# Kernel tuning notes

Measured on AMD Instinct MI355X. Metric: run time of the kernel, lower is better.

## Reference

```python
import jax, jax.numpy as jnp
import numpy as np

B, L, H, V, P = 256, 16, 256, 5000, 4
NPG, DEG, STEPS, OUT = 150, 4, 4, 2000
N, E = B * NPG, B * NPG * DEG


def _seg_softmax(x, seg, num):
    # sparse softmax over variable-size groups (rows of the sparse matrix)
    m = jax.ops.segment_max(x, seg, num_segments=num)
    e = jnp.exp(x - m[seg])
    s = jax.ops.segment_sum(e, seg, num_segments=num)
    return e / s[seg]


def setup_inputs():
    key = jax.random.key(0)
    ks = jax.random.split(key, 24)
    questions = jax.random.normal(ks[0], (B, L, H), jnp.float32)
    lengths = jax.random.randint(ks[1], (B,), L // 2, L + 1)
    node_attrs = jax.random.normal(ks[2], (N, P - 1, H), jnp.float32)
    edge_attrs = jax.random.normal(ks[3], (E, H), jnp.float32)
    node_graph = jnp.repeat(jnp.arange(B), NPG)
    edge_graph = jnp.repeat(jnp.arange(B), NPG * DEG)
    off = jnp.repeat(jnp.arange(B) * NPG, NPG * DEG)
    edge_src = jax.random.randint(ks[4], (E,), 0, NPG) + off
    edge_dst = jax.random.randint(ks[5], (E,), 0, NPG) + off
    s = float(1.0 / np.sqrt(H))
    u = lambda k, shape: jax.random.uniform(k, shape, jnp.float32, -s, s)
    vocab = jax.random.normal(ks[6], (V, H), jnp.float32) * 0.1
    default_embed = jax.random.uniform(ks[7], (H,), jnp.float32)
    W_norm = jnp.eye(H, dtype=jnp.float32)
    lstm_Wih, lstm_Whh = u(ks[8], (4 * H, H)), u(ks[9], (4 * H, H))
    lstm_bih, lstm_bhh = u(ks[10], (4 * H,)), u(ks[11], (4 * H,))
    rnn_Wih, rnn_Whh = u(ks[12], (H, H)), u(ks[13], (H, H))
    rnn_bih, rnn_bhh = u(ks[14], (H,)), u(ks[15], (H,))
    prop_embeds = jax.random.normal(ks[16], (P, H), jnp.float32) * 0.1
    Ws_property = jax.random.uniform(ks[17], (P, H, H), jnp.float32) * s
    W_state = jax.random.uniform(ks[18], (H,), jnp.float32) * s
    W_relation = jax.random.uniform(ks[19], (H,), jnp.float32) * s
    lin_W, lin_b = u(ks[20], (OUT, 2 * H)), u(ks[21], (OUT,))
    return dict(questions=questions, node_attrs=node_attrs, edge_attrs=edge_attrs,
                vocab=vocab, default_embed=default_embed, W_norm=W_norm,
                lstm_Wih=lstm_Wih, lstm_Whh=lstm_Whh, lstm_bih=lstm_bih, lstm_bhh=lstm_bhh,
                rnn_Wih=rnn_Wih, rnn_Whh=rnn_Whh, rnn_bih=rnn_bih, rnn_bhh=rnn_bhh,
                prop_embeds=prop_embeds, Ws_property=Ws_property,
                W_state=W_state, W_relation=W_relation, lin_W=lin_W, lin_b=lin_b,
                lengths=lengths, node_graph=node_graph, edge_graph=edge_graph,
                edge_src=edge_src, edge_dst=edge_dst)


def reference(questions, node_attrs, edge_attrs, vocab, default_embed, W_norm,
              lstm_Wih, lstm_Whh, lstm_bih, lstm_bhh,
              rnn_Wih, rnn_Whh, rnn_bih, rnn_bhh,
              prop_embeds, Ws_property, W_state, W_relation, lin_W, lin_b,
              lengths, node_graph, edge_graph, edge_src, edge_dst):
    # ---- NormalizeWordsModel (tagger) ----
    words = questions.reshape(B * L, H)
    C = jnp.concatenate([vocab, default_embed[None]], axis=0)  # [V+1, H]
    Pm = jax.nn.softmax((words @ W_norm) @ C.T, axis=1)        # [B*L, V+1]
    Vtag = Pm[:, -1:] * words + Pm[:, :-1] @ vocab             # [B*L, H]
    Vpad = Vtag.reshape(B, L, H)

    # ---- LSTM encoder: final hidden at last valid step (packed-sequence semantics) ----
    valid = jnp.arange(L)[:, None] < lengths[None, :]  # [L, B]

    def lstm_step(carry, inp):
        h, c = carry
        x, v = inp
        g = x @ lstm_Wih.T + lstm_bih + h @ lstm_Whh.T + lstm_bhh
        i, f, gc, o = jnp.split(g, 4, axis=-1)  # torch gate order i,f,g,o
        c_new = jax.nn.sigmoid(f) * c + jax.nn.sigmoid(i) * jnp.tanh(gc)
        h_new = jax.nn.sigmoid(o) * jnp.tanh(c_new)
        vm = v[:, None]
        return (jnp.where(vm, h_new, h), jnp.where(vm, c_new, c)), None

    z = jnp.zeros((B, H), questions.dtype)
    (Q, _), _ = jax.lax.scan(lstm_step, (z, z), (Vpad.transpose(1, 0, 2), valid))

    # ---- InstructionsDecoder: relu RNNCell fed the same Q each step ----
    def dec_step(hx, _):
        hx = jax.nn.relu(Q @ rnn_Wih.T + rnn_bih + hx @ rnn_Whh.T + rnn_bhh)
        return hx, hx

    _, Hins = jax.lax.scan(dec_step, z, None, length=STEPS)
    Hins = Hins.transpose(1, 0, 2)  # [B, STEPS, H]

    # ---- attention over (masked) tagged words ----
    att = jnp.einsum('bnh,blh->bnl', Hins, Vpad)
    mask = jnp.arange(L)[None, None, :] < lengths[:, None, None]
    att = jnp.where(mask, att, -jnp.inf)
    R = jax.nn.softmax(att, axis=-1) @ Vpad  # instructions [B, STEPS, H]

    # ---- NSMCell recurrence ----
    nodes_per_graph = jax.ops.segment_sum(jnp.ones(N, questions.dtype), node_graph, num_segments=B)
    dist = (1.0 / nodes_per_graph)[node_graph]  # [N]
    prop_sim = None
    for step in range(STEPS):
        instr = R[:, step]  # [B, H]
        prop_sim = jax.nn.softmax(instr @ prop_embeds.T, axis=1)  # [B, P]
        transformed = jnp.einsum('phk,npk->nph', Ws_property[:-1], node_attrs)  # [N, P-1, H]
        node_scores = jax.nn.elu(jnp.sum(
            prop_sim[node_graph, :-1, None] * instr[node_graph, None, :] * transformed, axis=1))  # [N, H]
        edge_scores = jax.nn.elu(instr[edge_graph] * (edge_attrs @ Ws_property[-1].T))  # [E, H]
        p_state = _seg_softmax(node_scores @ W_state, node_graph, B)  # [N]
        agg = jax.ops.segment_sum(dist[edge_src, None] * edge_scores, edge_dst, num_segments=N)  # [N, H]
        p_rel = _seg_softmax(agg @ W_relation, node_graph, B)  # [N]
        r = prop_sim[node_graph, -1]
        dist = r * p_rel + (1.0 - r) * p_state

    # ---- readout ----
    node_feat = jnp.sum(prop_sim[node_graph, :-1, None] * node_attrs, axis=1)  # [N, H]
    aggregated = jax.ops.segment_sum(dist[:, None] * node_feat, node_graph, num_segments=B)  # [B, H]
    return jnp.concatenate([Q, aggregated], axis=1) @ lin_W.T + lin_b
```

## Files before the change

### kernel.cpp

```cpp
#include <hip/hip_runtime.h>
#include <hip/hip_bf16.h>
#include <math.h>

#define BB 256
#define LL 16
#define HH 256
#define VV 5000
#define NPG 150
#define DEG 4
#define NSTEPS 4
#define OUTD 2000
#define NN (BB*NPG)
#define EE (BB*NPG*DEG)
#define BL (BB*LL)
#define VPAD 5120
#define KPAD 5024

__device__ __forceinline__ float wred_sum(float v){
  #pragma unroll
  for(int o=32;o;o>>=1) v += __shfl_down(v,o,64);
  return v;
}
__device__ __forceinline__ float wred_max(float v){
  #pragma unroll
  for(int o=32;o;o>>=1) v = fmaxf(v,__shfl_down(v,o,64));
  return v;
}
__device__ __forceinline__ float block_sum256(float v, float* sh){
  v = wred_sum(v);
  __syncthreads();
  if((threadIdx.x&63)==0) sh[threadIdx.x>>6]=v;
  __syncthreads();
  return sh[0]+sh[1]+sh[2]+sh[3];
}
__device__ __forceinline__ float block_max256(float v, float* sh){
  v = wred_max(v);
  __syncthreads();
  if((threadIdx.x&63)==0) sh[threadIdx.x>>6]=v;
  __syncthreads();
  return fmaxf(fmaxf(sh[0],sh[1]),fmaxf(sh[2],sh[3]));
}
__device__ __forceinline__ float eluf(float x){ return x>0.f ? x : expm1f(x); }
__device__ __forceinline__ float sigf(float x){ return 1.f/(1.f+expf(-x)); }
__device__ __forceinline__ float b2f(unsigned short s){
  union{float f; unsigned int u;} x; x.u = ((unsigned int)s)<<16; return x.f;
}
__device__ __forceinline__ unsigned short f2bf_bits(float x){
  union { __hip_bfloat16 h; unsigned short s; } u; u.h = __float2bfloat16(x); return u.s;
}

__device__ __forceinline__ void async16(void* lds, const void* g){
  __builtin_amdgcn_global_load_lds(
      (const __attribute__((address_space(1))) unsigned int*)g,
      (__attribute__((address_space(3))) unsigned int*)lds, 16, 0, 0);
}

typedef __attribute__((ext_vector_type(8))) short short8;
typedef __attribute__((ext_vector_type(4))) float f32x4;

__device__ __forceinline__ short8 pack8(float4 a, float4 b){
  short8 r;
  r[0]=(short)f2bf_bits(a.x); r[1]=(short)f2bf_bits(a.y);
  r[2]=(short)f2bf_bits(a.z); r[3]=(short)f2bf_bits(a.w);
  r[4]=(short)f2bf_bits(b.x); r[5]=(short)f2bf_bits(b.y);
  r[6]=(short)f2bf_bits(b.z); r[7]=(short)f2bf_bits(b.w);
  return r;
}

template<int EPI>
__global__ __launch_bounds__(256) void mfma_bt_bf16_k(
    const __hip_bfloat16* __restrict__ A, const __hip_bfloat16* __restrict__ Bt,
    float* __restrict__ Cf, __hip_bfloat16* __restrict__ Cb,
    int lda, int ldb, int ldc, int Nreal,
    int kItersTotal, int kPerSplit, const float* __restrict__ bias,
    const float* __restrict__ rscale)
{
  __shared__ __hip_bfloat16 As[128*32];
  __shared__ __hip_bfloat16 Bs[128*32];
  const int bm = blockIdx.y*128, bn = blockIdx.x*128;
  const int tid = threadIdx.x;
  int k0 = blockIdx.z * kPerSplit;
  int k1 = k0 + kPerSplit; if (k1 > kItersTotal) k1 = kItersTotal;
  const int lane = tid & 63, wave = tid >> 6;
  const int quad = lane >> 4, r16 = lane & 15;
  const int wr = wave >> 1, wc = wave & 1;
  f32x4 acc[4][4] = {};
  const int c0 = tid, c1 = tid + 256;
  const int ar0 = c0 >> 2, ak0 = (c0 & 3)*8;
  const int ar1 = c1 >> 2, ak1 = (c1 & 3)*8;
  const __hip_bfloat16* Ab = A + (size_t)bm*lda;
  const __hip_bfloat16* Bb = Bt + (size_t)bn*ldb;
  for (int kk = k0; kk < k1; ++kk){
    const int kb = kk*32;
    async16(&As[c0*8], Ab + (size_t)ar0*lda + kb + ak0);
    async16(&As[c1*8], Ab + (size_t)ar1*lda + kb + ak1);
    async16(&Bs[c0*8], Bb + (size_t)ar0*ldb + kb + ak0);
    async16(&Bs[c1*8], Bb + (size_t)ar1*ldb + kb + ak1);
    __syncthreads();
    short8 av[4], bv[4];
    #pragma unroll
    for (int i=0;i<4;i++){
      av[i] = *(const short8*)&As[(wr*64 + i*16 + r16)*32 + quad*8];
      bv[i] = *(const short8*)&Bs[(wc*64 + i*16 + r16)*32 + quad*8];
    }
    #pragma unroll
    for (int i=0;i<4;i++)
      #pragma unroll
      for (int j=0;j<4;j++)
        acc[i][j] = __builtin_amdgcn_mfma_f32_16x16x32_bf16(av[i], bv[j], acc[i][j], 0,0,0);
    __syncthreads();
  }
  #pragma unroll
  for (int i=0;i<4;i++){
    int row = bm + wr*64 + i*16 + quad*4;
    #pragma unroll
    for (int j=0;j<4;j++){
      int col = bn + wc*64 + j*16 + r16;
      if (col >= Nreal) continue;
      #pragma unroll
      for (int r=0;r<4;r++){
        float v = acc[i][j][r];
        if (EPI==0){ if (bias) v += bias[col]; Cf[(size_t)(row+r)*ldc + col] = v; }
        else if (EPI==1){ Cb[(size_t)(row+r)*ldc + col] = __float2bfloat16(v); }
        else { if (rscale) v *= rscale[row+r]; atomicAdd(&Cf[(size_t)(row+r)*ldc + col], v); }
      }
    }
  }
}

template<int EPI>
__global__ __launch_bounds__(256) void mfma_bt_f32_k(
    const float* __restrict__ A, const float* __restrict__ Bt,
    float* __restrict__ Cf, __hip_bfloat16* __restrict__ Cb,
    int lda, int ldb, int ldc, int Nreal,
    int kIters, const float* __restrict__ bias)
{
  __shared__ __hip_bfloat16 As[128*32];
  __shared__ __hip_bfloat16 Bs[128*32];
  const int bm = blockIdx.y*128, bn = blockIdx.x*128;
  const int tid = threadIdx.x;
  const int lane = tid & 63, wave = tid >> 6;
  const int quad = lane >> 4, r16 = lane & 15;
  const int wr = wave >> 1, wc = wave & 1;
  f32x4 acc[4][4] = {};
  for (int kk = 0; kk < kIters; ++kk){
    const int kb = kk*32;
    #pragma unroll
    for (int i=0;i<2;i++){
      int c = tid + i*256;
      int row = c >> 2, k0 = (c & 3)*8;
      const float* src = A + (size_t)(bm+row)*lda + kb + k0;
      float4 v0 = *(const float4*)(src);
      float4 v1 = *(const float4*)(src+4);
      *(short8*)&As[row*32 + k0] = pack8(v0, v1);
    }
    #pragma unroll
    for (int i=0;i<2;i++){
      int c = tid + i*256;
      int row = c >> 2, k0 = (c & 3)*8;
      float4 v0 = {0.f,0.f,0.f,0.f}, v1 = {0.f,0.f,0.f,0.f};
      if (bn + row < Nreal){
        const float* src = Bt + (size_t)(bn+row)*ldb + kb + k0;
        v0 = *(const float4*)(src);
        v1 = *(const float4*)(src+4);
      }
      *(short8*)&Bs[row*32 + k0] = pack8(v0, v1);
    }
    __syncthreads();
    short8 av[4], bv[4];
    #pragma unroll
    for (int i=0;i<4;i++){
      av[i] = *(const short8*)&As[(wr*64 + i*16 + r16)*32 + quad*8];
      bv[i] = *(const short8*)&Bs[(wc*64 + i*16 + r16)*32 + quad*8];
    }
    #pragma unroll
    for (int i=0;i<4;i++)
      #pragma unroll
      for (int j=0;j<4;j++)
        acc[i][j] = __builtin_amdgcn_mfma_f32_16x16x32_bf16(av[i], bv[j], acc[i][j], 0,0,0);
    __syncthreads();
  }
  #pragma unroll
  for (int i=0;i<4;i++){
    int row = bm + wr*64 + i*16 + quad*4;
    #pragma unroll
    for (int j=0;j<4;j++){
      int col = bn + wc*64 + j*16 + r16;
      if (col >= Nreal) continue;
      #pragma unroll
      for (int r=0;r<4;r++){
        float v = acc[i][j][r];
        if (EPI==0){ if (bias) v += bias[col]; Cf[(size_t)(row+r)*ldc + col] = v; }
        else { Cb[(size_t)(row+r)*ldc + col] = __float2bfloat16(v); }
      }
    }
  }
}

__global__ __launch_bounds__(256) void gemm_exp_k(
    const __hip_bfloat16* __restrict__ A, const __hip_bfloat16* __restrict__ Bt,
    __hip_bfloat16* __restrict__ Pm, float* __restrict__ row_sum,
    float* __restrict__ e_def)
{
  __shared__ __hip_bfloat16 As[128*32];
  __shared__ __hip_bfloat16 Bs[128*32];
  const int bm = blockIdx.y*128, bn = blockIdx.x*128;
  const int tid = threadIdx.x;
  const int lane = tid & 63, wave = tid >> 6;
  const int quad = lane >> 4, r16 = lane & 15;
  const int wr = wave >> 1, wc = wave & 1;
  f32x4 acc[4][4] = {};
  const int c0 = tid, c1 = tid + 256;
  const int ar0 = c0 >> 2, ak0 = (c0 & 3)*8;
  const int ar1 = c1 >> 2, ak1 = (c1 & 3)*8;
  const __hip_bfloat16* Ab = A + (size_t)bm*HH;
  const __hip_bfloat16* Bb = Bt + (size_t)bn*HH;
  for (int kk = 0; kk < HH/32; ++kk){
    const int kb = kk*32;
    async16(&As[c0*8], Ab + (size_t)ar0*HH + kb + ak0);
    async16(&As[c1*8], Ab + (size_t)ar1*HH + kb + ak1);
    async16(&Bs[c0*8], Bb + (size_t)ar0*HH + kb + ak0);
    async16(&Bs[c1*8], Bb + (size_t)ar1*HH + kb + ak1);
    __syncthreads();
    short8 av[4], bv[4];
    #pragma unroll
    for (int i=0;i<4;i++){
      av[i] = *(const short8*)&As[(wr*64 + i*16 + r16)*32 + quad*8];
      bv[i] = *(const short8*)&Bs[(wc*64 + i*16 + r16)*32 + quad*8];
    }
    #pragma unroll
    for (int i=0;i<4;i++)
      #pragma unroll
      for (int j=0;j<4;j++)
        acc[i][j] = __builtin_amdgcn_mfma_f32_16x16x32_bf16(av[i], bv[j], acc[i][j], 0,0,0);
    __syncthreads();
  }
  #pragma unroll
  for (int i=0;i<4;i++){
    int rowb = bm + wr*64 + i*16 + quad*4;
    float rsum[4] = {0.f,0.f,0.f,0.f};
    #pragma unroll
    for (int j=0;j<4;j++){
      int col = bn + wc*64 + j*16 + r16;
      #pragma unroll
      for (int r=0;r<4;r++){
        float e = (col <= VV) ? expf(acc[i][j][r]) : 0.f;
        rsum[r] += e;
        if (col < KPAD) Pm[(size_t)(rowb+r)*KPAD + col] = __float2bfloat16(col < VV ? e : 0.f);
        if (col == VV) e_def[rowb+r] = e;
      }
    }
    #pragma unroll
    for (int r=0;r<4;r++){
      float s = rsum[r];
      s += __shfl_xor(s, 1, 64);
      s += __shfl_xor(s, 2, 64);
      s += __shfl_xor(s, 4, 64);
      s += __shfl_xor(s, 8, 64);
      if (r16 == 0) atomicAdd(&row_sum[rowb+r], s);
    }
  }
}

__global__ __launch_bounds__(1024) void lstm_persist_k(
    const float* __restrict__ gX, const __hip_bfloat16* __restrict__ Whh_bf,
    const int* __restrict__ lengths,
    float* __restrict__ h_out, __hip_bfloat16* __restrict__ hbf_out)
{
  __shared__ __hip_bfloat16 Wl[256*264];
  __shared__ __hip_bfloat16 hbuf[2][16*264];
  __shared__ int len_s[16];
  const int bg = blockIdx.x, tid = threadIdx.x;
  const int lane = tid & 63, w = tid >> 6;
  const int quad = lane >> 4, r16 = lane & 15;
  const int hb = w*16;
  for (int c = tid; c < 8192; c += 1024){
    int row = c >> 5, ci = (c & 31)*8;
    int g = row >> 6, rr = row & 63;
    *(short8*)&Wl[row*264 + ci] = *(const short8*)&Whh_bf[((size_t)(g*256+rr))*256 + ci];
  }
  for (int i = tid; i < 16*264; i += 1024) hbuf[0][i] = __float2bfloat16(0.f);
  if (tid < 16) len_s[tid] = lengths[bg*16 + tid];
  __syncthreads();
  int lenr[4];
  #pragma unroll
  for (int r=0;r<4;r++) lenr[r] = len_s[quad*4 + r];
  f32x4 cstate = {0.f,0.f,0.f,0.f};
  f32x4 hstate = {0.f,0.f,0.f,0.f};
  int p = 0;
  for (int t=0; t<LL; t++){
    f32x4 acc[4] = {};
    const __hip_bfloat16* hr = hbuf[p];
    if (w < 4){
      #pragma unroll
      for (int kc=0; kc<8; kc++){
        short8 a = *(const short8*)&hr[r16*264 + kc*32 + quad*8];
        #pragma unroll
        for (int g=0; g<4; g++){
          short8 b = *(const short8*)&Wl[(g*64 + hb + r16)*264 + kc*32 + quad*8];
          acc[g] = __builtin_amdgcn_mfma_f32_16x16x32_bf16(a, b, acc[g], 0,0,0);
        }
      }
    } else {
      #pragma unroll
      for (int kc=0; kc<8; kc++){
        short8 a = *(const short8*)&hr[r16*264 + kc*32 + quad*8];
        #pragma unroll
        for (int g=0; g<4; g++){
          short8 b = *(const short8*)&Whh_bf[((size_t)(g*256 + hb + r16))*256 + kc*32 + quad*8];
          acc[g] = __builtin_amdgcn_mfma_f32_16x16x32_bf16(a, b, acc[g], 0,0,0);
        }
      }
    }
    #pragma unroll
    for (int r=0;r<4;r++){
      int batch = quad*4 + r;
      const float* gx = gX + ((size_t)((bg*16+batch)*LL + t))*(4*HH) + hb + r16;
      float gi = acc[0][r] + gx[0];
      float gf = acc[1][r] + gx[HH];
      float gc = acc[2][r] + gx[2*HH];
      float go = acc[3][r] + gx[3*HH];
      float cn = sigf(gf)*cstate[r] + sigf(gi)*tanhf(gc);
      float hn = sigf(go)*tanhf(cn);
      if (t < lenr[r]){ cstate[r] = cn; hstate[r] = hn; }
      hbuf[p^1][batch*264 + hb + r16] = __float2bfloat16(hstate[r]);
    }
    p ^= 1;
    __syncthreads();
  }
  #pragma unroll
  for (int r=0;r<4;r++){
    int batch = quad*4 + r;
    size_t o = (size_t)(bg*16+batch)*HH + hb + r16;
    h_out[o] = hstate[r];
    hbf_out[o] = __float2bfloat16(hstate[r]);
  }
}

__global__ __launch_bounds__(1024) void dec_persist_k(
    const __hip_bfloat16* __restrict__ Qbf, const __hip_bfloat16* __restrict__ Wih_bf,
    const __hip_bfloat16* __restrict__ Whh_bf,
    const float* __restrict__ bih, const float* __restrict__ bhh,
    float* __restrict__ Hins)
{
  __shared__ __hip_bfloat16 Wl[256*264];
  __shared__ __hip_bfloat16 xb[2][16*264];
  const int bg = blockIdx.x, tid = threadIdx.x;
  const int lane = tid & 63, w = tid >> 6;
  const int quad = lane >> 4, r16 = lane & 15;
  const int col = w*16 + r16;
  for (int c = tid; c < 8192; c += 1024){
    int row = c >> 5, ci = (c & 31)*8;
    *(short8*)&Wl[row*264 + ci] = *(const short8*)&Whh_bf[(size_t)row*256 + ci];
  }
  f32x4 qp = {};
  #pragma unroll
  for (int kc=0; kc<8; kc++){
    short8 a = *(const short8*)&Qbf[(size_t)(bg*16 + r16)*HH + kc*32 + quad*8];
    short8 b = *(const short8*)&Wih_bf[(size_t)col*HH + kc*32 + quad*8];
    qp = __builtin_amdgcn_mfma_f32_16x16x32_bf16(a, b, qp, 0,0,0);
  }
  const float bihv = bih[col], bhhv = bhh[col];
  __syncthreads();
  #pragma unroll
  for (int r=0;r<4;r++){
    int batch = quad*4 + r;
    float v = fmaxf(qp[r] + bihv + bhhv, 0.f);
    xb[0][batch*264 + col] = __float2bfloat16(v);
    Hins[(size_t)(bg*16+batch)*(NSTEPS*HH) + 0*HH + col] = v;
  }
  __syncthreads();
  int p = 0;
  for (int s=1; s<NSTEPS; s++){
    f32x4 acc = {};
    #pragma unroll
    for (int kc=0; kc<8; kc++){
      short8 a = *(const short8*)&xb[p][r16*264 + kc*32 + quad*8];
      short8 b = *(const short8*)&Wl[col*264 + kc*32 + quad*8];
      acc = __builtin_amdgcn_mfma_f32_16x16x32_bf16(a, b, acc, 0,0,0);
    }
    #pragma unroll
    for (int r=0;r<4;r++){
      int batch = quad*4 + r;
      float v = fmaxf(qp[r] + bihv + acc[r] + bhhv, 0.f);
      xb[p^1][batch*264 + col] = __float2bfloat16(v);
      Hins[(size_t)(bg*16+batch)*(NSTEPS*HH) + s*HH + col] = v;
    }
    p ^= 1;
    __syncthreads();
  }
}

__global__ void cvt_bf16_k(const float* __restrict__ src, __hip_bfloat16* __restrict__ dst, int n){
  int i = (blockIdx.x*256 + threadIdx.x)*4;
  if (i >= n) return;
  float4 v = *(const float4*)(src + i);
  dst[i]   = __float2bfloat16(v.x);
  dst[i+1] = __float2bfloat16(v.y);
  dst[i+2] = __float2bfloat16(v.z);
  dst[i+3] = __float2bfloat16(v.w);
}

__global__ void tr_cvt_k(const float* __restrict__ src, __hip_bfloat16* __restrict__ dst, int R, int Ccols){
  int idx = blockIdx.x*256 + threadIdx.x;
  if (idx >= R*Ccols) return;
  int r = idx / Ccols, c = idx % Ccols;
  dst[(size_t)c*R + r] = __float2bfloat16(src[idx]);
}

__global__ void build_cb_k(const float* __restrict__ vocab, const float* __restrict__ de,
                           __hip_bfloat16* __restrict__ Cb){
  int idx = blockIdx.x*256 + threadIdx.x;
  if (idx >= VPAD*HH) return;
  int v = idx >> 8, h = idx & 255;
  float x = (v < VV) ? vocab[(size_t)v*HH + h] : (v == VV ? de[h] : 0.f);
  Cb[idx] = __float2bfloat16(x);
}

__global__ void build_vt_k(const float* __restrict__ vocab, __hip_bfloat16* __restrict__ VT){
  int idx = blockIdx.x*256 + threadIdx.x;
  if (idx >= HH*KPAD) return;
  int h = idx / KPAD, v = idx % KPAD;
  VT[idx] = __float2bfloat16(v < VV ? vocab[(size_t)v*HH + h] : 0.f);
}

__global__ void bsum_k(const float* a, const float* b, float* o){
  int i = blockIdx.x*256 + threadIdx.x;
  if (i < 4*HH) o[i] = a[i] + b[i];
}

__global__ void init_k(float* dist, float* s_rel){
  int idx = blockIdx.x*256 + threadIdx.x;
  if (idx < NN){ dist[idx] = 1.f/150.f; s_rel[idx] = 0.f; }
}

__global__ void zero_k(float* p, int n){
  int idx = blockIdx.x*256 + threadIdx.x;
  if (idx < n) p[idx] = 0.f;
}

__global__ void inv_k(float* p, int n){
  int idx = blockIdx.x*256 + threadIdx.x;
  if (idx < n) p[idx] = 1.f/p[idx];
}

__global__ void vtag_epi_k(float* __restrict__ Vtag, const float* __restrict__ e_def,
                           const float* __restrict__ inv_s, const float* __restrict__ words){
  int r = blockIdx.x, h = threadIdx.x;
  size_t o = (size_t)r*HH + h;
  Vtag[o] += e_def[r]*inv_s[r]*words[o];
}

__global__ __launch_bounds__(256) void attention_k(const float* __restrict__ Vtag,
                                                   const float* __restrict__ Hins,
                                                   const int* __restrict__ lengths,
                                                   float* __restrict__ R){
  __shared__ float Vl[LL][HH];
  __shared__ float Hn[NSTEPS][HH];
  __shared__ float att[NSTEPS][LL];
  int b = blockIdx.x, tid = threadIdx.x;
  for (int idx=tid; idx<LL*HH; idx+=256){ int l=idx>>8, h=idx&255; Vl[l][h] = Vtag[((size_t)b*LL+l)*HH + h]; }
  for (int idx=tid; idx<NSTEPS*HH; idx+=256){ Hn[idx>>8][idx&255] = Hins[(size_t)b*(NSTEPS*HH) + idx]; }
  __syncthreads();
  if (tid < NSTEPS*LL){
    int n2 = tid>>4, l = tid&15;
    float s = 0.f;
    for (int k=0;k<HH;k++) s += Hn[n2][k]*Vl[l][k];
    att[n2][l] = s;
  }
  __syncthreads();
  int len = lengths[b];
  if (tid < NSTEPS){
    float m = -1e30f;
    for (int l=0;l<len;l++) m = fmaxf(m, att[tid][l]);
    float s = 0.f;
    for (int l=0;l<LL;l++){ float e = (l<len)? expf(att[tid][l]-m) : 0.f; att[tid][l]=e; s+=e; }
    float inv = 1.f/s;
    for (int l=0;l<LL;l++) att[tid][l] *= inv;
  }
  __syncthreads();
  {
    int n2 = tid>>6, h0 = (tid&63)*4;
    float r0=0,r1=0,r2=0,r3=0;
    for (int l=0;l<LL;l++){
      float w = att[n2][l];
      r0 += w*Vl[l][h0]; r1 += w*Vl[l][h0+1]; r2 += w*Vl[l][h0+2]; r3 += w*Vl[l][h0+3];
    }
    float* o = R + (size_t)b*(NSTEPS*HH) + n2*HH + h0;
    o[0]=r0; o[1]=r1; o[2]=r2; o[3]=r3;
  }
}

__global__ __launch_bounds__(256) void prop_sim_all_k(const float* __restrict__ R,
                                                      const float* __restrict__ pe,
                                                      float* __restrict__ psa){
  __shared__ float sp[4];
  int gb = blockIdx.x;
  int s = gb >> 8, b = gb & 255;
  int tid = threadIdx.x;
  int p = tid>>6, lane = tid&63;
  const float* instr = R + (size_t)b*(NSTEPS*HH) + s*HH;
  float v = 0.f;
  for (int h=lane; h<HH; h+=64) v += instr[h]*pe[p*HH+h];
  v = wred_sum(v);
  if (lane==0) sp[p] = v;
  __syncthreads();
  if (tid==0){
    float m = fmaxf(fmaxf(sp[0],sp[1]),fmaxf(sp[2],sp[3]));
    float e0=expf(sp[0]-m), e1=expf(sp[1]-m), e2=expf(sp[2]-m), e3=expf(sp[3]-m);
    float ss = e0+e1+e2+e3;
    float* o = psa + (size_t)s*BB*4 + b*4;
    o[0]=e0/ss; o[1]=e1/ss; o[2]=e2/ss; o[3]=e3/ss;
  }
}

__global__ __launch_bounds__(256) void nsm_scores_k(
    const __hip_bfloat16* __restrict__ Tf, const __hip_bfloat16* __restrict__ ET,
    const float* __restrict__ R, const float* __restrict__ psa_s,
    const float* __restrict__ W_state, const float* __restrict__ Wr,
    const float* __restrict__ dist, const int* __restrict__ esrc, const int* __restrict__ edst,
    float* __restrict__ s_state, float* __restrict__ s_rel, int step)
{
  const int wave = threadIdx.x >> 6, lane = threadIdx.x & 63;
  const int h0 = lane*4;
  if (blockIdx.x < NN/4){
    int n = blockIdx.x*4 + wave;
    int g = n / NPG;
    const float* instr = R + (size_t)g*(NSTEPS*HH) + step*HH;
    float ps0 = psa_s[g*4], ps1 = psa_s[g*4+1], ps2 = psa_s[g*4+2];
    const unsigned short* t = (const unsigned short*)(Tf + (size_t)n*(3*HH));
    ushort4 t0 = *(const ushort4*)(t + h0);
    ushort4 t1 = *(const ushort4*)(t + HH + h0);
    ushort4 t2 = *(const ushort4*)(t + 2*HH + h0);
    float4 iv = *(const float4*)(instr + h0);
    float4 wv = *(const float4*)(W_state + h0);
    float acc;
    acc  = eluf(iv.x*(ps0*b2f(t0.x)+ps1*b2f(t1.x)+ps2*b2f(t2.x)))*wv.x;
    acc += eluf(iv.y*(ps0*b2f(t0.y)+ps1*b2f(t1.y)+ps2*b2f(t2.y)))*wv.y;
    acc += eluf(iv.z*(ps0*b2f(t0.z)+ps1*b2f(t1.z)+ps2*b2f(t2.z)))*wv.z;
    acc += eluf(iv.w*(ps0*b2f(t0.w)+ps1*b2f(t1.w)+ps2*b2f(t2.w)))*wv.w;
    acc = wred_sum(acc);
    if (lane==0) s_state[n] = acc;
  } else {
    int e = (blockIdx.x - NN/4)*4 + wave;
    int b = e / (NPG*DEG);
    const float* instr = R + (size_t)b*(NSTEPS*HH) + step*HH;
    const unsigned short* et = (const unsigned short*)(ET + (size_t)e*HH);
    ushort4 ev = *(const ushort4*)(et + h0);
    float4 iv = *(const float4*)(instr + h0);
    float4 wv = *(const float4*)(Wr + h0);
    float acc;
    acc  = eluf(iv.x*b2f(ev.x))*wv.x;
    acc += eluf(iv.y*b2f(ev.y))*wv.y;
    acc += eluf(iv.z*b2f(ev.z))*wv.z;
    acc += eluf(iv.w*b2f(ev.w))*wv.w;
    acc = wred_sum(acc);
    if (lane==0) atomicAdd(&s_rel[edst[e]], dist[esrc[e]]*acc);
  }
}

__global__ __launch_bounds__(256) void nsm_update_k(
    const float* __restrict__ s_state, float* __restrict__ s_rel,
    const float* __restrict__ psa_s, float* __restrict__ dist)
{
  __shared__ float sh[4];
  int b = blockIdx.x, i = threadIdx.x;
  bool ok = (i < NPG);
  float ss = ok ? s_state[b*NPG + i] : -1e30f;
  float sr = ok ? s_rel[b*NPG + i]   : -1e30f;
  float m1 = block_max256(ss, sh);
  float e1 = ok ? expf(ss - m1) : 0.f;
  float d1 = block_sum256(e1, sh);
  float m2 = block_max256(sr, sh);
  float e2 = ok ? expf(sr - m2) : 0.f;
  float d2 = block_sum256(e2, sh);
  if (ok){
    float pst = e1/d1, prl = e2/d2;
    float r = psa_s[b*4+3];
    dist[b*NPG + i] = r*prl + (1.f-r)*pst;
    s_rel[b*NPG + i] = 0.f;
  }
}

__global__ __launch_bounds__(256) void final_agg_k(const float* __restrict__ na, const float* __restrict__ dist,
                                                   const float* __restrict__ ps, float* __restrict__ aggregated){
  int b = blockIdx.x, h = threadIdx.x;
  float ps0 = ps[b*4+0], ps1 = ps[b*4+1], ps2 = ps[b*4+2];
  float acc = 0.f;
  for (int i=0;i<NPG;i++){
    int n = b*NPG + i;
    float d = dist[n];
    const float* a = na + (size_t)n*(3*HH);
    acc += d*(ps0*a[h] + ps1*a[HH+h] + ps2*a[2*HH+h]);
  }
  aggregated[b*HH + h] = acc;
}

__global__ void qa_build_k(const float* __restrict__ Q, const float* __restrict__ aggregated,
                           float* __restrict__ QA){
  int idx = blockIdx.x*256 + threadIdx.x;
  if (idx >= BB*2*HH) return;
  int b = idx >> 9, k = idx & 511;
  QA[idx] = (k < HH) ? Q[b*HH + k] : aggregated[b*HH + (k-HH)];
}

extern "C" void kernel_launch(void* const* d_in, const int* in_sizes, int n_in,
                              void* d_out, int out_size, void* d_ws, size_t ws_size,
                              hipStream_t stream) {
  (void)in_sizes; (void)n_in; (void)out_size; (void)ws_size;
  const float* questions     = (const float*)d_in[0];
  const float* node_attrs    = (const float*)d_in[1];
  const float* edge_attrs    = (const float*)d_in[2];
  const float* vocab         = (const float*)d_in[3];
  const float* default_embed = (const float*)d_in[4];
  const float* W_norm        = (const float*)d_in[5];
  const float* lstm_Wih      = (const float*)d_in[6];
  const float* lstm_Whh      = (const float*)d_in[7];
  const float* lstm_bih      = (const float*)d_in[8];
  const float* lstm_bhh      = (const float*)d_in[9];
  const float* rnn_Wih       = (const float*)d_in[10];
  const float* rnn_Whh       = (const float*)d_in[11];
  const float* rnn_bih       = (const float*)d_in[12];
  const float* rnn_bhh       = (const float*)d_in[13];
  const float* prop_embeds   = (const float*)d_in[14];
  const float* Ws_property   = (const float*)d_in[15];
  const float* W_state       = (const float*)d_in[16];
  const float* W_relation    = (const float*)d_in[17];
  const float* lin_W         = (const float*)d_in[18];
  const float* lin_b         = (const float*)d_in[19];
  const int*   lengths       = (const int*)d_in[20];
  const int*   edge_src      = (const int*)d_in[23];
  const int*   edge_dst      = (const int*)d_in[24];
  float* out = (float*)d_out;

  char* base = (char*)d_ws;
  size_t off = 0;
  auto alloc = [&](size_t nbytes)->void*{
    void* p = base + off;
    off += (nbytes + 255) & ~(size_t)255;
    return p;
  };

  __hip_bfloat16* qbf     = (__hip_bfloat16*)alloc((size_t)BL*HH*2);
  __hip_bfloat16* WnT_bf  = (__hip_bfloat16*)alloc((size_t)HH*HH*2);
  __hip_bfloat16* xw_bf   = (__hip_bfloat16*)alloc((size_t)BL*HH*2);
  __hip_bfloat16* Cbv     = (__hip_bfloat16*)alloc((size_t)VPAD*HH*2);
  __hip_bfloat16* vT_bf   = (__hip_bfloat16*)alloc((size_t)HH*KPAD*2);
  __hip_bfloat16* Whh_bf  = (__hip_bfloat16*)alloc((size_t)4*HH*HH*2);
  __hip_bfloat16* rWih_bf = (__hip_bfloat16*)alloc((size_t)HH*HH*2);
  __hip_bfloat16* rWhh_bf = (__hip_bfloat16*)alloc((size_t)HH*HH*2);
  __hip_bfloat16* h_bf    = (__hip_bfloat16*)alloc((size_t)BB*HH*2);
  float* e_def    = (float*)alloc((size_t)BL*4);
  float* row_sum  = (float*)alloc((size_t)BL*4);
  float* Vtag     = (float*)alloc((size_t)BL*HH*4);
  float* bsum     = (float*)alloc((size_t)4*HH*4);
  float* h_buf    = (float*)alloc((size_t)BB*HH*4);
  float* Hins     = (float*)alloc((size_t)BB*NSTEPS*HH*4);
  float* R        = (float*)alloc((size_t)BB*NSTEPS*HH*4);
  float* psa      = (float*)alloc((size_t)NSTEPS*BB*4*4);
  float* s_state  = (float*)alloc((size_t)NN*4);
  float* s_rel    = (float*)alloc((size_t)NN*4);
  float* dist     = (float*)alloc((size_t)NN*4);
  float* aggregated = (float*)alloc((size_t)BB*HH*4);
  float* QA       = (float*)alloc((size_t)BB*2*HH*4);
  __hip_bfloat16* Pm_bf = (__hip_bfloat16*)alloc((size_t)BL*KPAD*2);
  char*  TfR      = (char*)alloc((size_t)NN*3*HH*2);
  __hip_bfloat16* Tf = (__hip_bfloat16*)TfR;
  float* gX          = (float*)TfR;
  __hip_bfloat16* ET = (__hip_bfloat16*)alloc((size_t)EE*HH*2);

  init_k<<<(NN+255)/256, 256, 0, stream>>>(dist, s_rel);
  cvt_bf16_k<<<(BL*HH/4+255)/256, 256, 0, stream>>>(questions, qbf, BL*HH);
  tr_cvt_k<<<(HH*HH+255)/256, 256, 0, stream>>>(W_norm, WnT_bf, HH, HH);
  build_cb_k<<<(VPAD*HH+255)/256, 256, 0, stream>>>(vocab, default_embed, Cbv);
  build_vt_k<<<(HH*KPAD+255)/256, 256, 0, stream>>>(vocab, vT_bf);
  cvt_bf16_k<<<(4*HH*HH/4+255)/256, 256, 0, stream>>>(lstm_Whh, Whh_bf, 4*HH*HH);
  cvt_bf16_k<<<(HH*HH/4+255)/256, 256, 0, stream>>>(rnn_Wih, rWih_bf, HH*HH);
  cvt_bf16_k<<<(HH*HH/4+255)/256, 256, 0, stream>>>(rnn_Whh, rWhh_bf, HH*HH);
  bsum_k<<<(4*HH+255)/256, 256, 0, stream>>>(lstm_bih, lstm_bhh, bsum);
  zero_k<<<(BL+255)/256, 256, 0, stream>>>(row_sum, BL);
  zero_k<<<(BL*HH+255)/256, 256, 0, stream>>>(Vtag, BL*HH);

  mfma_bt_bf16_k<1><<<dim3(2,32,1), 256, 0, stream>>>(qbf, WnT_bf, nullptr, xw_bf,
      HH, HH, HH, HH, HH/32, HH/32, nullptr, nullptr);
  gemm_exp_k<<<dim3(VPAD/128, BL/128, 1), 256, 0, stream>>>(xw_bf, Cbv, Pm_bf, row_sum, e_def);
  inv_k<<<(BL+255)/256, 256, 0, stream>>>(row_sum, BL);
  mfma_bt_bf16_k<2><<<dim3(HH/128, BL/128, 8), 256, 0, stream>>>(
      Pm_bf, vT_bf, Vtag, nullptr, KPAD, KPAD, HH, HH, KPAD/32, 20, nullptr, row_sum);
  vtag_epi_k<<<BL, HH, 0, stream>>>(Vtag, e_def, row_sum, questions);

  mfma_bt_f32_k<0><<<dim3(8,32,1), 256, 0, stream>>>(Vtag, lstm_Wih, gX, nullptr,
      HH, HH, 4*HH, 4*HH, HH/32, bsum);
  lstm_persist_k<<<16, 1024, 0, stream>>>(gX, Whh_bf, lengths, h_buf, h_bf);

  dec_persist_k<<<16, 1024, 0, stream>>>(h_bf, rWih_bf, rWhh_bf, rnn_bih, rnn_bhh, Hins);

  attention_k<<<BB, 256, 0, stream>>>(Vtag, Hins, lengths, R);
  prop_sim_all_k<<<NSTEPS*BB, 256, 0, stream>>>(R, prop_embeds, psa);

  for (int p=0; p<3; p++)
    mfma_bt_f32_k<1><<<dim3(2,NN/128,1), 256, 0, stream>>>(
        node_attrs + (size_t)p*HH, Ws_property + (size_t)p*HH*HH,
        nullptr, Tf + (size_t)p*HH, 3*HH, HH, 3*HH, HH, HH/32, nullptr);
  mfma_bt_f32_k<1><<<dim3(2,EE/128,1), 256, 0, stream>>>(
      edge_attrs, Ws_property + (size_t)3*HH*HH,
      nullptr, ET, HH, HH, HH, HH, HH/32, nullptr);

  for (int s=0; s<NSTEPS; s++){
    const float* psa_s = psa + (size_t)s*BB*4;
    nsm_scores_k<<<NN/4 + EE/4, 256, 0, stream>>>(
        Tf, ET, R, psa_s, W_state, W_relation, dist, edge_src, edge_dst,
        s_state, s_rel, s);
    nsm_update_k<<<BB, 256, 0, stream>>>(s_state, s_rel, psa_s, dist);
  }

  final_agg_k<<<BB, 256, 0, stream>>>(node_attrs, dist, psa + (size_t)3*BB*4, aggregated);
  qa_build_k<<<(BB*2*HH+255)/256, 256, 0, stream>>>(h_buf, aggregated, QA);
  mfma_bt_f32_k<0><<<dim3(16,2,1), 256, 0, stream>>>(QA, lin_W, out, nullptr,
      2*HH, 2*HH, OUTD, OUTD, 2*HH/32, lin_b);
}
```

Measured before the change: 1.152 ms.

## Split LSTM recurrent weights across registers, LDS and global; use fast sigmoid/tanh

Restructures the persistent LSTM kernel's Whh placement. Each warp now holds the first three K-chunks of its weights in registers, six warps keep the remaining chunks in LDS, and only the other warps still read from global memory. Previously only four warps used LDS. The gate inputs gX are loaded at the top of each timestep ahead of the MFMAs to hide latency, and sigmoid/tanh switch to fast rcp/__expf approximations. The cost is higher register pressure at 1024 threads and slightly lower accuracy in the activations.

```diff
diff --git a/kernel.cpp b/kernel.cpp
--- a/kernel.cpp
+++ b/kernel.cpp
@@ -42,6 +42,12 @@
 }
 __device__ __forceinline__ float eluf(float x){ return x>0.f ? x : expm1f(x); }
 __device__ __forceinline__ float sigf(float x){ return 1.f/(1.f+expf(-x)); }
+__device__ __forceinline__ float fsig(float x){
+  return __builtin_amdgcn_rcpf(1.f + __expf(-x));
+}
+__device__ __forceinline__ float ftanh(float x){
+  return 1.f - 2.f*__builtin_amdgcn_rcpf(1.f + __expf(2.f*x));
+}
 __device__ __forceinline__ float b2f(unsigned short s){
   union{float f; unsigned int u;} x; x.u = ((unsigned int)s)<<16; return x.f;
 }
@@ -267,43 +273,62 @@
     const int* __restrict__ lengths,
     float* __restrict__ h_out, __hip_bfloat16* __restrict__ hbf_out)
 {
-  __shared__ __hip_bfloat16 Wl[256*264];
+  __shared__ __hip_bfloat16 Wl[384*164];
   __shared__ __hip_bfloat16 hbuf[2][16*264];
-  __shared__ int len_s[16];
   const int bg = blockIdx.x, tid = threadIdx.x;
   const int lane = tid & 63, w = tid >> 6;
   const int quad = lane >> 4, r16 = lane & 15;
   const int hb = w*16;
-  for (int c = tid; c < 8192; c += 1024){
-    int row = c >> 5, ci = (c & 31)*8;
-    int g = row >> 6, rr = row & 63;
-    *(short8*)&Wl[row*264 + ci] = *(const short8*)&Whh_bf[((size_t)(g*256+rr))*256 + ci];
-  }
+  for (int idx = tid; idx < 384*20; idx += 1024){
+    int row = idx / 20, c8 = (idx % 20)*8;
+    int ww = row >> 6, g = (row >> 4) & 3, rr = row & 15;
+    *(short8*)&Wl[row*164 + c8] =
+        *(const short8*)&Whh_bf[((size_t)(g*256 + ww*16 + rr))*256 + 96 + c8];
+  }
+  short8 rW[3][4];
+  #pragma unroll
+  for (int kc=0; kc<3; kc++)
+    #pragma unroll
+    for (int g=0; g<4; g++)
+      rW[kc][g] = *(const short8*)&Whh_bf[((size_t)(g*256 + hb + r16))*256 + kc*32 + quad*8];
   for (int i = tid; i < 16*264; i += 1024) hbuf[0][i] = __float2bfloat16(0.f);
-  if (tid < 16) len_s[tid] = lengths[bg*16 + tid];
-  __syncthreads();
   int lenr[4];
   #pragma unroll
-  for (int r=0;r<4;r++) lenr[r] = len_s[quad*4 + r];
+  for (int r=0;r<4;r++) lenr[r] = lengths[bg*16 + quad*4 + r];
+  __syncthreads();
   f32x4 cstate = {0.f,0.f,0.f,0.f};
   f32x4 hstate = {0.f,0.f,0.f,0.f};
   int p = 0;
+  const float* gXb = gX + (size_t)bg*16*LL*(4*HH) + hb + r16;
   for (int t=0; t<LL; t++){
+    float gxv[4][4];
+    #pragma unroll
+    for (int r=0;r<4;r++)
+      #pragma unroll
+      for (int g=0;g<4;g++)
+        gxv[r][g] = gXb[((size_t)((quad*4+r)*LL + t))*(4*HH) + g*HH];
     f32x4 acc[4] = {};
     const __hip_bfloat16* hr = hbuf[p];
-    if (w < 4){
-      #pragma unroll
-      for (int kc=0; kc<8; kc++){
+    #pragma unroll
+    for (int kc=0; kc<3; kc++){
+      short8 a = *(const short8*)&hr[r16*264 + kc*32 + quad*8];
+      #pragma unroll
+      for (int g=0; g<4; g++)
+        acc[g] = __builtin_amdgcn_mfma_f32_16x16x32_bf16(a, rW[kc][g], acc[g], 0,0,0);
+    }
+    if (w < 6){
+      #pragma unroll
+      for (int kc=3; kc<8; kc++){
         short8 a = *(const short8*)&hr[r16*264 + kc*32 + quad*8];
         #pragma unroll
         for (int g=0; g<4; g++){
-          short8 b = *(const short8*)&Wl[(g*64 + hb + r16)*264 + kc*32 + quad*8];
+          short8 b = *(const short8*)&Wl[(w*64 + g*16 + r16)*164 + (kc-3)*32 + quad*8];
           acc[g] = __builtin_amdgcn_mfma_f32_16x16x32_bf16(a, b, acc[g], 0,0,0);
         }
       }
     } else {
       #pragma unroll
-      for (int kc=0; kc<8; kc++){
+      for (int kc=3; kc<8; kc++){
         short8 a = *(const short8*)&hr[r16*264 + kc*32 + quad*8];
         #pragma unroll
         for (int g=0; g<4; g++){
@@ -315,13 +340,12 @@
     #pragma unroll
     for (int r=0;r<4;r++){
       int batch = quad*4 + r;
-      const float* gx = gX + ((size_t)((bg*16+batch)*LL + t))*(4*HH) + hb + r16;
-      float gi = acc[0][r] + gx[0];
-      float gf = acc[1][r] + gx[HH];
-      float gc = acc[2][r] + gx[2*HH];
-      float go = acc[3][r] + gx[3*HH];
-      float cn = sigf(gf)*cstate[r] + sigf(gi)*tanhf(gc);
-      float hn = sigf(go)*tanhf(cn);
+      float gi = acc[0][r] + gxv[r][0];
+      float gf = acc[1][r] + gxv[r][1];
+      float gc = acc[2][r] + gxv[r][2];
+      float go = acc[3][r] + gxv[r][3];
+      float cn = fsig(gf)*cstate[r] + fsig(gi)*ftanh(gc);
+      float hn = fsig(go)*ftanh(cn);
       if (t < lenr[r]){ cstate[r] = cn; hstate[r] = hn; }
       hbuf[p^1][batch*264 + hb + r16] = __float2bfloat16(hstate[r]);
     }
```

New measurement: 1.100 ms. -4.5%, faster.
